# Optimization experiments

Measured on AMD Instinct MI355X. Metric: run time of the kernel, lower is better.

Reference implementation:

```python
import jax, jax.numpy as jnp
import numpy as np

B, T, C, H = 2, 2048, 1024, 16
HS = C // H                      # head_size = 64
LAYER_IDX = 2
LAMBDA_INIT = 0.8 - 0.6 * float(np.exp(-0.3 * (LAYER_IDX - 1)))
EPS = 1e-12


def setup_inputs() -> dict:
    key = jax.random.key(0)
    ks = jax.random.split(key, 22)
    std = 0.02
    w = lambda k, shape: (jax.random.normal(k, shape, jnp.float32) * std)
    inp = {
        'q': jax.random.normal(ks[0], (B, T, C), jnp.float32),
        'k': jax.random.normal(ks[1], (B, T, C), jnp.float32),
        'v': jax.random.normal(ks[2], (B, T, C), jnp.float32),
        'mask': jax.random.randint(ks[3], (B, T), 0, 2).astype(jnp.int32),
        # projection weights stored as (in, out) so y = x @ W + b
        'Wq1': w(ks[4], (C, C)), 'bq1': jnp.zeros((C,), jnp.float32),
        'Wq2': w(ks[5], (C, C)), 'bq2': jnp.zeros((C,), jnp.float32),
        'Wk1': w(ks[6], (C, C)), 'bk1': jnp.zeros((C,), jnp.float32),
        'Wk2': w(ks[7], (C, C)), 'bk2': jnp.zeros((C,), jnp.float32),
        'Wv':  w(ks[8], (C, 2 * C)), 'bv': jnp.zeros((2 * C,), jnp.float32),
        'Wc':  w(ks[9], (2 * C, C)), 'bc': jnp.zeros((C,), jnp.float32),
        'ln_w': jnp.ones((2 * HS,), jnp.float32),
        'ln_b': jnp.zeros((2 * HS,), jnp.float32),
        'lq1': jax.random.normal(ks[10], (H, HS), jnp.float32) * 0.1,
        'lk1': jax.random.normal(ks[11], (H, HS), jnp.float32) * 0.1,
        'lq2': jax.random.normal(ks[12], (H, HS), jnp.float32) * 0.1,
        'lk2': jax.random.normal(ks[13], (H, HS), jnp.float32) * 0.1,
    }
    return inp


def reference(q, k, v, mask, Wq1, bq1, Wq2, bq2, Wk1, bk1, Wk2, bk2,
              Wv, bv, Wc, bc, ln_w, ln_b, lq1, lk1, lq2, lk2):
    def heads(x, d):  # [B,T,H*d] -> [B,H,T,d]
        return x.reshape(B, T, H, d).transpose(0, 2, 1, 3)

    q1 = heads(q @ Wq1 + bq1, HS)
    q2 = heads(q @ Wq2 + bq2, HS)
    k1 = heads(k @ Wk1 + bk1, HS)
    k2 = heads(k @ Wk2 + bk2, HS)
    vv = heads(v @ Wv + bv, 2 * HS)          # [B,H,T,2*HS]

    scale = 1.0 / np.sqrt(HS)
    att1 = jnp.einsum('bhqd,bhkd->bhqk', q1, k1) * scale
    att2 = jnp.einsum('bhqd,bhkd->bhqk', q2, k2) * scale

    m = (mask == 0)[:, None, :, None]         # [B,1,Tq,1] -> masks query rows
    att1 = jnp.where(m, -1e9, att1)
    att2 = jnp.where(m, -1e9, att2)
    att1 = jax.nn.softmax(att1, axis=-1)
    att2 = jax.nn.softmax(att2, axis=-1)

    lam1 = jnp.exp(jnp.sum(lq1 * lk1, axis=-1))   # [H]
    lam2 = jnp.exp(jnp.sum(lq2 * lk2, axis=-1))
    lam = (lam1 - lam2 + LAMBDA_INIT)[None, :, None, None]
    att = att1 - lam * att2                       # differential attention

    y = jnp.einsum('bhqk,bhkd->bhqd', att, vv)    # [B,H,T,2*HS]

    # per-head TF-style LayerNorm over 2*HS, then (1 - lambda_init) scale
    u = y.mean(-1, keepdims=True)
    s = ((y - u) ** 2).mean(-1, keepdims=True)
    y = ln_w * ((y - u) / jnp.sqrt(s + EPS)) + ln_b
    y = y * (1.0 - LAMBDA_INIT)

    y = y.transpose(0, 2, 1, 3).reshape(B, T, 2 * C)
    return y @ Wc + bc
```

## Files before the change

### kernel.cpp

```cpp
#include <hip/hip_runtime.h>
#include <hip/hip_bf16.h>
#include <stdint.h>


#define T_SEQ 2048

typedef unsigned short u16;
typedef __attribute__((ext_vector_type(8))) short short8;
typedef __attribute__((ext_vector_type(4))) float f32x4;
typedef __attribute__((ext_vector_type(16))) float f32x16;

#define LAMBDA_INIT 0.35550906759096926f
#define ONE_MINUS_LI 0.6444909324090307f
#define SM_SCALE 0.125f
#define LOG2E 1.44269504f

__device__ __forceinline__ u16 f2bf(float f) {
  uint32_t u = __float_as_uint(f);
  return (u16)((u + 0x7FFFu + ((u >> 16) & 1u)) >> 16);
}
__device__ __forceinline__ float b2f(u16 u) {
  return __uint_as_float(((uint32_t)u) << 16);
}
__device__ __forceinline__ short8 ld8(const u16* p) {
  return *reinterpret_cast<const short8*>(p);
}
__device__ __forceinline__ void st8(u16* p, short8 v) {
  *reinterpret_cast<short8*>(p) = v;
}
__device__ __forceinline__ f32x4 mfma16(short8 a, short8 b, f32x4 c) {
  return __builtin_amdgcn_mfma_f32_16x16x32_bf16(a, b, c, 0, 0, 0);
}
__device__ __forceinline__ f32x16 mfma32(short8 a, short8 b, f32x16 c) {
  return __builtin_amdgcn_mfma_f32_32x32x16_bf16(a, b, c, 0, 0, 0);
}
__device__ __forceinline__ uint32_t cvtpk(float lo, float hi_) {
  uint32_t r;
  asm("v_cvt_pk_bf16_f32 %0, %1, %2" : "=v"(r) : "v"(lo), "v"(hi_));
  return r;
}

__global__ __launch_bounds__(256) void cvt_bf16(const float* __restrict__ in,
                                                u16* __restrict__ out, int n) {
  int i = (blockIdx.x * 256 + threadIdx.x) * 4;
  if (i >= n) return;
  float4 f = *reinterpret_cast<const float4*>(in + i);
  union { u16 u[4]; uint2 v; } pk;
  pk.u[0] = f2bf(f.x); pk.u[1] = f2bf(f.y); pk.u[2] = f2bf(f.z); pk.u[3] = f2bf(f.w);
  *reinterpret_cast<uint2*>(out + i) = pk.v;
}

__global__ __launch_bounds__(256) void tcvt(const float* __restrict__ W,
                                            u16* __restrict__ WT,
                                            int K, int N, int outRowOff) {
  __shared__ float tile[32][33];
  int n0 = blockIdx.x * 32, k0 = blockIdx.y * 32;
  int tx = threadIdx.x & 31, ty = threadIdx.x >> 5;
#pragma unroll
  for (int p = 0; p < 4; ++p)
    tile[ty + 8 * p][tx] = W[(size_t)(k0 + ty + 8 * p) * N + n0 + tx];
  __syncthreads();
#pragma unroll
  for (int p = 0; p < 4; ++p)
    WT[(size_t)(outRowOff + n0 + ty + 8 * p) * K + k0 + tx] = f2bf(tile[tx][ty + 8 * p]);
}

__global__ __launch_bounds__(256) void bias_concat(const float* __restrict__ b1,
                                                   const float* __restrict__ b2,
                                                   float* __restrict__ out) {
  int i = blockIdx.x * 256 + threadIdx.x;
  out[i] = (i < 1024) ? b1[i] : b2[i - 1024];
}

#define BM 128
#define BN 128
#define BK 64

template <int EPI>
__global__ __launch_bounds__(256) void gemm_bt(const u16* __restrict__ A,
                                               const u16* __restrict__ BT,
                                               const float* __restrict__ bias,
                                               void* __restrict__ Cv,
                                               int M, int N, int K) {
  __shared__ __align__(16) u16 As[BM * BK];
  __shared__ __align__(16) u16 Bs[BN * BK];
  int t = threadIdx.x;
  int w = t >> 6, l = t & 63;
  int g = l >> 4, c16 = l & 15;
  int wr = w >> 1, wc = w & 1;
  size_t gm = (size_t)blockIdx.y * BM, gn = (size_t)blockIdx.x * BN;

  f32x4 acc[4][4] = {};

  int srow = l >> 3;
  int scol = (l & 7) * 8;
  const u16* Ag = A + (gm + w * 32 + srow) * (size_t)K + scol;
  const u16* Bg = BT + (gn + w * 32 + srow) * (size_t)K + scol;

  for (int kt = 0; kt < K; kt += BK) {
    __syncthreads();
#pragma unroll
    for (int c = 0; c < 4; ++c) {
      __builtin_amdgcn_global_load_lds(
          (const __attribute__((address_space(1))) void*)(Ag + (size_t)(c * 8) * K + kt),
          (__attribute__((address_space(3))) void*)&As[(w * 32 + c * 8) * BK], 16, 0, 0);
      __builtin_amdgcn_global_load_lds(
          (const __attribute__((address_space(1))) void*)(Bg + (size_t)(c * 8) * K + kt),
          (__attribute__((address_space(3))) void*)&Bs[(w * 32 + c * 8) * BK], 16, 0, 0);
    }
    __syncthreads();
#pragma unroll
    for (int kk = 0; kk < 2; ++kk) {
      short8 af[4], bf[4];
#pragma unroll
      for (int m = 0; m < 4; ++m)
        af[m] = *reinterpret_cast<const short8*>(
            &As[(wr * 64 + m * 16 + c16) * BK + kk * 32 + g * 8]);
#pragma unroll
      for (int n = 0; n < 4; ++n)
        bf[n] = *reinterpret_cast<const short8*>(
            &Bs[(wc * 64 + n * 16 + c16) * BK + kk * 32 + g * 8]);
#pragma unroll
      for (int m = 0; m < 4; ++m)
#pragma unroll
        for (int n = 0; n < 4; ++n)
          acc[m][n] = mfma16(af[m], bf[n], acc[m][n]);
    }
  }

#pragma unroll
  for (int m = 0; m < 4; ++m)
#pragma unroll
    for (int n = 0; n < 4; ++n) {
      int row0 = (int)gm + wr * 64 + m * 16 + g * 4;
      int col = (int)gn + wc * 64 + n * 16 + c16;
      float bz = bias[col];
      if (EPI == 0) {
        u16* C = (u16*)Cv;
#pragma unroll
        for (int r = 0; r < 4; ++r)
          C[(size_t)(row0 + r) * N + col] = f2bf(acc[m][n][r] + bz);
      } else if (EPI == 1) {
        u16* C = (u16*)Cv;
        int bb = row0 >> 11, tt = row0 & 2047;
        union { u16 u[4]; uint2 v; } pk;
#pragma unroll
        for (int r = 0; r < 4; ++r) pk.u[r] = f2bf(acc[m][n][r] + bz);
        *reinterpret_cast<uint2*>(&C[((size_t)(bb * 2048 + col)) * 2048 + tt]) = pk.v;
      } else {
        float* C = (float*)Cv;
#pragma unroll
        for (int r = 0; r < 4; ++r)
          C[(size_t)(row0 + r) * N + col] = acc[m][n][r] + bz;
      }
    }
}

#define KROW 72
#define VROW 40
#define YROW 72
__global__ __launch_bounds__(256, 3) void diffattn(
    const u16* __restrict__ q1q2, const u16* __restrict__ k1k2,
    const u16* __restrict__ vvT, const int* __restrict__ mask,
    const float* __restrict__ lq1, const float* __restrict__ lk1,
    const float* __restrict__ lq2, const float* __restrict__ lk2,
    const float* __restrict__ lnw, const float* __restrict__ lnb,
    u16* __restrict__ yout) {
  __shared__ __align__(16) u16 smem[9728];
  u16* Ksm = smem;
  u16* Vsm = smem + 4608;
  u16* Ysm = smem;

  int tid = threadIdx.x;
  int w = tid >> 6, l = tid & 63;
  int q = l & 31, hi = l >> 5;
  int pair = w >> 1, stream = w & 1;

  int id = blockIdx.x;
  int j = id & 7, rest = id >> 3;
  int xblk = rest & 31, ygrp = rest >> 5;
  int bh = ygrp * 8 + j;
  int b = bh >> 4, h = bh & 15;
  int qr0 = xblk * 64 + pair * 32;

  float lm1 = lq1[h * 64 + l] * lk1[h * 64 + l];
  float lm2 = lq2[h * 64 + l] * lk2[h * 64 + l];
#pragma unroll
  for (int o = 32; o; o >>= 1) {
    lm1 += __shfl_xor(lm1, o);
    lm2 += __shfl_xor(lm2, o);
  }
  float lam = __expf(lm1) - __expf(lm2) + LAMBDA_INIT;

  int soff = stream * 1024;
  const u16* qrow = q1q2 + (size_t)(b * T_SEQ + qr0 + q) * 2048 + h * 64 + soff + hi * 8;
  short8 qf[4];
#pragma unroll
  for (int c = 0; c < 4; ++c) qf[c] = ld8(qrow + c * 16);

  float scale = (mask[b * T_SEQ + qr0 + q] == 0) ? 0.f : (SM_SCALE * LOG2E);

  float M = -INFINITY, L = 0.f;
  f32x16 acc[4] = {};

  int ku = tid * 2;
  int krow = ku >> 3, kslot = ku & 7;
  int kstream = krow >> 5, kkey = krow & 31;
  const u16* srcK = k1k2 + (size_t)(b * T_SEQ + kkey) * 2048 + h * 64 + kstream * 1024 + kslot * 8;
  u16* dstK = &Ksm[(kstream * 32 + kkey) * KROW + kslot * 8];
  int vd = tid >> 1, vslot = (tid & 1) * 2;
  const u16* srcV = vvT + ((size_t)(b * 16 + h) * 128 + vd) * 2048 + vslot * 8;
  u16* dstV = &Vsm[vd * VROW + vslot * 8];

  short8 kr0 = ld8(srcK), kr1 = ld8(srcK + 8);
  short8 vr0 = ld8(srcV), vr1 = ld8(srcV + 8);

  for (int kt = 0; kt < T_SEQ; kt += 32) {
    __syncthreads();
    st8(dstK, kr0); st8(dstK + 8, kr1);
    st8(dstV, vr0); st8(dstV + 8, vr1);
    __syncthreads();
    if (kt + 32 < T_SEQ) {
      const u16* nk = srcK + (size_t)(kt + 32) * 2048;
      kr0 = ld8(nk); kr1 = ld8(nk + 8);
      const u16* nv = srcV + (kt + 32);
      vr0 = ld8(nv); vr1 = ld8(nv + 8);
    }

    const u16* kbase = &Ksm[(stream * 32 + q) * KROW + hi * 8];
    short8 kf[4];
#pragma unroll
    for (int c = 0; c < 4; ++c) kf[c] = ld8(kbase + c * 16);

    f32x16 s = {};
#pragma unroll
    for (int c = 0; c < 4; ++c) s = mfma32(kf[c], qf[c], s);

    float rm = fmaxf(fmaxf(s[0], s[1]), s[2]);
    rm = fmaxf(fmaxf(rm, s[3]), s[4]);
    rm = fmaxf(fmaxf(rm, s[5]), s[6]);
    rm = fmaxf(fmaxf(rm, s[7]), s[8]);
    rm = fmaxf(fmaxf(rm, s[9]), s[10]);
    rm = fmaxf(fmaxf(rm, s[11]), s[12]);
    rm = fmaxf(fmaxf(rm, s[13]), s[14]);
    rm = fmaxf(rm, s[15]);
    rm = fmaxf(rm, __shfl_xor(rm, 32));
    float tm = rm * scale;

    if (!__all(tm - M <= 11.5f)) {
      float Mn = fmaxf(M, tm);
      float a = exp2f(M - Mn);
      L *= a;
#pragma unroll
      for (int d = 0; d < 4; ++d) acc[d] *= a;
      M = Mn;
    }

    float p[16];
#pragma unroll
    for (int r = 0; r < 16; ++r) p[r] = exp2f(__builtin_fmaf(s[r], scale, -M));
    float s8[8], s4[4];
#pragma unroll
    for (int i = 0; i < 8; ++i) s8[i] = p[i] + p[i + 8];
#pragma unroll
    for (int i = 0; i < 4; ++i) s4[i] = s8[i] + s8[i + 4];
    float ps = (s4[0] + s4[1]) + (s4[2] + s4[3]);
    ps += __shfl_xor(ps, 32);
    L += ps;

    uint32_t a1 = cvtpk(p[0], p[1]), a2 = cvtpk(p[2], p[3]);
    uint32_t b1 = cvtpk(p[4], p[5]), b2 = cvtpk(p[6], p[7]);
    uint32_t c1 = cvtpk(p[8], p[9]), c2 = cvtpk(p[10], p[11]);
    uint32_t d1 = cvtpk(p[12], p[13]), d2 = cvtpk(p[14], p[15]);
    uint32_t sa1 = (uint32_t)__shfl_xor((int)a1, 32), sa2 = (uint32_t)__shfl_xor((int)a2, 32);
    uint32_t sb1 = (uint32_t)__shfl_xor((int)b1, 32), sb2 = (uint32_t)__shfl_xor((int)b2, 32);
    uint32_t sc1 = (uint32_t)__shfl_xor((int)c1, 32), sc2 = (uint32_t)__shfl_xor((int)c2, 32);
    uint32_t sd1 = (uint32_t)__shfl_xor((int)d1, 32), sd2 = (uint32_t)__shfl_xor((int)d2, 32);
    union { uint32_t u[4]; short8 s8v; } pu0, pu1;
    pu0.u[0] = hi ? sb1 : a1;  pu0.u[1] = hi ? sb2 : a2;
    pu0.u[2] = hi ? b1 : sa1;  pu0.u[3] = hi ? b2 : sa2;
    pu1.u[0] = hi ? sd1 : c1;  pu1.u[1] = hi ? sd2 : c2;
    pu1.u[2] = hi ? d1 : sc1;  pu1.u[3] = hi ? d2 : sc2;
    short8 pf0 = pu0.s8v, pf1 = pu1.s8v;

#pragma unroll
    for (int d = 0; d < 4; ++d) {
      const u16* vb0 = &Vsm[(d * 32 + q) * VROW + hi * 8];
      short8 vf0 = ld8(vb0);
      short8 vf1 = ld8(vb0 + 16);
      acc[d] = mfma32(vf0, pf0, acc[d]);
      acc[d] = mfma32(vf1, pf1, acc[d]);
    }
  }

  float inv = 1.f / L;
  __syncthreads();
  if (stream == 1) {
    u16* yrow = &Ysm[(pair * 64 + l) * YROW];
#pragma unroll
    for (int d = 0; d < 4; ++d) {
      union { uint32_t u[8]; short8 v[2]; } pk;
#pragma unroll
      for (int i = 0; i < 8; ++i)
        pk.u[i] = cvtpk(acc[d][2 * i] * inv, acc[d][2 * i + 1] * inv);
      st8(yrow + d * 16, pk.v[0]);
      st8(yrow + d * 16 + 8, pk.v[1]);
    }
  }
  __syncthreads();
  if (stream == 0) {
    const u16* yrow = &Ysm[(pair * 64 + l) * YROW];
    float y[4][16];
#pragma unroll
    for (int d = 0; d < 4; ++d) {
      short8 y2a = ld8(yrow + d * 16);
      short8 y2b = ld8(yrow + d * 16 + 8);
#pragma unroll
      for (int i = 0; i < 8; ++i) {
        y[d][i] = acc[d][i] * inv - lam * b2f((u16)y2a[i]);
        y[d][8 + i] = acc[d][8 + i] * inv - lam * b2f((u16)y2b[i]);
      }
    }
    float sm = 0.f;
#pragma unroll
    for (int d = 0; d < 4; ++d)
#pragma unroll
      for (int r = 0; r < 16; ++r) sm += y[d][r];
    sm += __shfl_xor(sm, 32);
    float u = sm * (1.f / 128.f);
    float var = 0.f;
#pragma unroll
    for (int d = 0; d < 4; ++d)
#pragma unroll
      for (int r = 0; r < 16; ++r) { float dd = y[d][r] - u; var += dd * dd; }
    var += __shfl_xor(var, 32);
    float rstd = rsqrtf(var * (1.f / 128.f) + 1e-12f);

    size_t orow = (size_t)(b * T_SEQ + qr0 + q) * 2048 + h * 128;
#pragma unroll
    for (int d = 0; d < 4; ++d)
#pragma unroll
      for (int rr = 0; rr < 4; ++rr) {
        int base = d * 32 + 8 * rr + 4 * hi;
        union { u16 u[4]; uint2 v; } o;
#pragma unroll
        for (int i = 0; i < 4; ++i) {
          float yv = (lnw[base + i] * ((y[d][rr * 4 + i] - u) * rstd) + lnb[base + i]) *
                     ONE_MINUS_LI;
          o.u[i] = f2bf(yv);
        }
        *reinterpret_cast<uint2*>(&yout[orow + base]) = o.v;
      }
  }
}

extern "C" void kernel_launch(void* const* d_in, const int* in_sizes, int n_in,
                              void* d_out, int out_size, void* d_ws, size_t ws_size,
                              hipStream_t stream) {
  (void)in_sizes; (void)n_in; (void)out_size; (void)ws_size;
  const float* q   = (const float*)d_in[0];
  const float* k   = (const float*)d_in[1];
  const float* v   = (const float*)d_in[2];
  const int* maskp = (const int*)d_in[3];
  const float* Wq1 = (const float*)d_in[4];
  const float* bq1 = (const float*)d_in[5];
  const float* Wq2 = (const float*)d_in[6];
  const float* bq2 = (const float*)d_in[7];
  const float* Wk1 = (const float*)d_in[8];
  const float* bk1 = (const float*)d_in[9];
  const float* Wk2 = (const float*)d_in[10];
  const float* bk2 = (const float*)d_in[11];
  const float* Wv  = (const float*)d_in[12];
  const float* bv  = (const float*)d_in[13];
  const float* Wc  = (const float*)d_in[14];
  const float* bc  = (const float*)d_in[15];
  const float* lnw = (const float*)d_in[16];
  const float* lnb = (const float*)d_in[17];
  const float* lq1 = (const float*)d_in[18];
  const float* lk1 = (const float*)d_in[19];
  const float* lq2 = (const float*)d_in[20];
  const float* lk2 = (const float*)d_in[21];

  char* ws = (char*)d_ws;
  u16* qb     = (u16*)(ws + 0);
  u16* kb     = (u16*)(ws + 8388608);
  u16* vb     = (u16*)(ws + 16777216);
  u16* Wq12T  = (u16*)(ws + 25165824);
  u16* Wk12T  = (u16*)(ws + 29360128);
  u16* WvT    = (u16*)(ws + 33554432);
  u16* WcT    = (u16*)(ws + 37748736);
  float* biasq = (float*)(ws + 41943040);
  float* biask = (float*)(ws + 41951232);
  u16* q1q2   = (u16*)(ws + 41959424);
  u16* k1k2   = (u16*)(ws + 58736640);
  u16* vvT    = (u16*)(ws + 75513856);
  u16* yb     = (u16*)(ws + 0);

  const int NELEM = 2 * T_SEQ * 1024;

  cvt_bf16<<<4096, 256, 0, stream>>>(q, qb, NELEM);
  cvt_bf16<<<4096, 256, 0, stream>>>(k, kb, NELEM);
  cvt_bf16<<<4096, 256, 0, stream>>>(v, vb, NELEM);

  tcvt<<<dim3(32, 32), 256, 0, stream>>>(Wq1, Wq12T, 1024, 1024, 0);
  tcvt<<<dim3(32, 32), 256, 0, stream>>>(Wq2, Wq12T, 1024, 1024, 1024);
  tcvt<<<dim3(32, 32), 256, 0, stream>>>(Wk1, Wk12T, 1024, 1024, 0);
  tcvt<<<dim3(32, 32), 256, 0, stream>>>(Wk2, Wk12T, 1024, 1024, 1024);
  tcvt<<<dim3(64, 32), 256, 0, stream>>>(Wv, WvT, 1024, 2048, 0);
  tcvt<<<dim3(32, 64), 256, 0, stream>>>(Wc, WcT, 2048, 1024, 0);

  bias_concat<<<8, 256, 0, stream>>>(bq1, bq2, biasq);
  bias_concat<<<8, 256, 0, stream>>>(bk1, bk2, biask);

  gemm_bt<0><<<dim3(16, 32), 256, 0, stream>>>(qb, Wq12T, biasq, q1q2, 4096, 2048, 1024);
  gemm_bt<0><<<dim3(16, 32), 256, 0, stream>>>(kb, Wk12T, biask, k1k2, 4096, 2048, 1024);
  gemm_bt<1><<<dim3(16, 32), 256, 0, stream>>>(vb, WvT, bv, vvT, 4096, 2048, 1024);

  diffattn<<<1024, 256, 0, stream>>>(q1q2, k1k2, vvT, maskp,
                                     lq1, lk1, lq2, lk2, lnw, lnb, yb);

  gemm_bt<2><<<dim3(8, 32), 256, 0, stream>>>(yb, WcT, bc, d_out, 4096, 1024, 2048);
}
```

Before: 330.0 us.

## Merge Q/K projection GEMMs and stage 64-key K/V tiles in attention

The Q and K projection GEMMs become one launch over 8192 rows. Blocks in the second half offset the weight and bias pointers, which relies on the Q/K buffers, weights and biases sitting contiguously in the workspace. The attention kernel now stages 64 keys of K and V per barrier pair instead of 32, processing two 32-key sub-tiles per stage. This halves the syncthreads and prefetch rounds per key. In exchange, LDS per block roughly doubles and more registers are held in prefetch buffers, which may limit occupancy.

```diff
diff --git a/kernel.cpp b/kernel.cpp
--- a/kernel.cpp
+++ b/kernel.cpp
@@ -76,7 +76,7 @@
 #define BN 128
 #define BK 64
 
-template <int EPI>
+template <int EPI, bool QK>
 __global__ __launch_bounds__(256) void gemm_bt(const u16* __restrict__ A,
                                                const u16* __restrict__ BT,
                                                const float* __restrict__ bias,
@@ -89,6 +89,10 @@
   int g = l >> 4, c16 = l & 15;
   int wr = w >> 1, wc = w & 1;
   size_t gm = (size_t)blockIdx.y * BM, gn = (size_t)blockIdx.x * BN;
+  if (QK && gm >= 4096) {
+    BT += (size_t)2048 * 1024;
+    bias += 2048;
+  }
 
   f32x4 acc[4][4] = {};
 
@@ -157,7 +161,6 @@
 }
 
 #define KROW 72
-#define VROW 40
 #define YROW 72
 __global__ __launch_bounds__(256, 3) void diffattn(
     const u16* __restrict__ q1q2, const u16* __restrict__ k1k2,
@@ -166,9 +169,9 @@
     const float* __restrict__ lq2, const float* __restrict__ lk2,
     const float* __restrict__ lnw, const float* __restrict__ lnb,
     u16* __restrict__ yout) {
-  __shared__ __align__(16) u16 smem[9728];
+  __shared__ __align__(16) u16 smem[18432];
   u16* Ksm = smem;
-  u16* Vsm = smem + 4608;
+  u16* Vsm = smem + 9216;
   u16* Ysm = smem;
 
   int tid = threadIdx.x;
@@ -203,93 +206,105 @@
   float M = -INFINITY, L = 0.f;
   f32x16 acc[4] = {};
 
-  int ku = tid * 2;
-  int krow = ku >> 3, kslot = ku & 7;
-  int kstream = krow >> 5, kkey = krow & 31;
-  const u16* srcK = k1k2 + (size_t)(b * T_SEQ + kkey) * 2048 + h * 64 + kstream * 1024 + kslot * 8;
-  u16* dstK = &Ksm[(kstream * 32 + kkey) * KROW + kslot * 8];
-  int vd = tid >> 1, vslot = (tid & 1) * 2;
-  const u16* srcV = vvT + ((size_t)(b * 16 + h) * 128 + vd) * 2048 + vslot * 8;
-  u16* dstV = &Vsm[vd * VROW + vslot * 8];
-
-  short8 kr0 = ld8(srcK), kr1 = ld8(srcK + 8);
-  short8 vr0 = ld8(srcV), vr1 = ld8(srcV + 8);
-
-  for (int kt = 0; kt < T_SEQ; kt += 32) {
+  int srw = tid >> 1, shalf = tid & 1;
+  int kstream = srw >> 6, kkey = srw & 63;
+  const u16* srcK =
+      k1k2 + (size_t)(b * T_SEQ + kkey) * 2048 + h * 64 + kstream * 1024 + shalf * 32;
+  u16* dstK = &Ksm[srw * KROW + shalf * 32];
+  const u16* srcV = vvT + ((size_t)(b * 16 + h) * 128 + srw) * 2048 + shalf * 32;
+  u16* dstV = &Vsm[srw * KROW + shalf * 32];
+
+  short8 kpre[4], vpre[4];
+#pragma unroll
+  for (int u = 0; u < 4; ++u) {
+    kpre[u] = ld8(srcK + u * 8);
+    vpre[u] = ld8(srcV + u * 8);
+  }
+
+  for (int kt = 0; kt < T_SEQ; kt += 64) {
     __syncthreads();
-    st8(dstK, kr0); st8(dstK + 8, kr1);
-    st8(dstV, vr0); st8(dstV + 8, vr1);
+#pragma unroll
+    for (int u = 0; u < 4; ++u) {
+      st8(dstK + u * 8, kpre[u]);
+      st8(dstV + u * 8, vpre[u]);
+    }
     __syncthreads();
-    if (kt + 32 < T_SEQ) {
-      const u16* nk = srcK + (size_t)(kt + 32) * 2048;
-      kr0 = ld8(nk); kr1 = ld8(nk + 8);
-      const u16* nv = srcV + (kt + 32);
-      vr0 = ld8(nv); vr1 = ld8(nv + 8);
-    }
-
-    const u16* kbase = &Ksm[(stream * 32 + q) * KROW + hi * 8];
-    short8 kf[4];
-#pragma unroll
-    for (int c = 0; c < 4; ++c) kf[c] = ld8(kbase + c * 16);
-
-    f32x16 s = {};
-#pragma unroll
-    for (int c = 0; c < 4; ++c) s = mfma32(kf[c], qf[c], s);
-
-    float rm = fmaxf(fmaxf(s[0], s[1]), s[2]);
-    rm = fmaxf(fmaxf(rm, s[3]), s[4]);
-    rm = fmaxf(fmaxf(rm, s[5]), s[6]);
-    rm = fmaxf(fmaxf(rm, s[7]), s[8]);
-    rm = fmaxf(fmaxf(rm, s[9]), s[10]);
-    rm = fmaxf(fmaxf(rm, s[11]), s[12]);
-    rm = fmaxf(fmaxf(rm, s[13]), s[14]);
-    rm = fmaxf(rm, s[15]);
-    rm = fmaxf(rm, __shfl_xor(rm, 32));
-    float tm = rm * scale;
-
-    if (!__all(tm - M <= 11.5f)) {
-      float Mn = fmaxf(M, tm);
-      float a = exp2f(M - Mn);
-      L *= a;
-#pragma unroll
-      for (int d = 0; d < 4; ++d) acc[d] *= a;
-      M = Mn;
-    }
-
-    float p[16];
-#pragma unroll
-    for (int r = 0; r < 16; ++r) p[r] = exp2f(__builtin_fmaf(s[r], scale, -M));
-    float s8[8], s4[4];
-#pragma unroll
-    for (int i = 0; i < 8; ++i) s8[i] = p[i] + p[i + 8];
-#pragma unroll
-    for (int i = 0; i < 4; ++i) s4[i] = s8[i] + s8[i + 4];
-    float ps = (s4[0] + s4[1]) + (s4[2] + s4[3]);
-    ps += __shfl_xor(ps, 32);
-    L += ps;
-
-    uint32_t a1 = cvtpk(p[0], p[1]), a2 = cvtpk(p[2], p[3]);
-    uint32_t b1 = cvtpk(p[4], p[5]), b2 = cvtpk(p[6], p[7]);
-    uint32_t c1 = cvtpk(p[8], p[9]), c2 = cvtpk(p[10], p[11]);
-    uint32_t d1 = cvtpk(p[12], p[13]), d2 = cvtpk(p[14], p[15]);
-    uint32_t sa1 = (uint32_t)__shfl_xor((int)a1, 32), sa2 = (uint32_t)__shfl_xor((int)a2, 32);
-    uint32_t sb1 = (uint32_t)__shfl_xor((int)b1, 32), sb2 = (uint32_t)__shfl_xor((int)b2, 32);
-    uint32_t sc1 = (uint32_t)__shfl_xor((int)c1, 32), sc2 = (uint32_t)__shfl_xor((int)c2, 32);
-    uint32_t sd1 = (uint32_t)__shfl_xor((int)d1, 32), sd2 = (uint32_t)__shfl_xor((int)d2, 32);
-    union { uint32_t u[4]; short8 s8v; } pu0, pu1;
-    pu0.u[0] = hi ? sb1 : a1;  pu0.u[1] = hi ? sb2 : a2;
-    pu0.u[2] = hi ? b1 : sa1;  pu0.u[3] = hi ? b2 : sa2;
-    pu1.u[0] = hi ? sd1 : c1;  pu1.u[1] = hi ? sd2 : c2;
-    pu1.u[2] = hi ? d1 : sc1;  pu1.u[3] = hi ? d2 : sc2;
-    short8 pf0 = pu0.s8v, pf1 = pu1.s8v;
-
-#pragma unroll
-    for (int d = 0; d < 4; ++d) {
-      const u16* vb0 = &Vsm[(d * 32 + q) * VROW + hi * 8];
-      short8 vf0 = ld8(vb0);
-      short8 vf1 = ld8(vb0 + 16);
-      acc[d] = mfma32(vf0, pf0, acc[d]);
-      acc[d] = mfma32(vf1, pf1, acc[d]);
+    if (kt + 64 < T_SEQ) {
+      const u16* nk = srcK + (size_t)(kt + 64) * 2048;
+      const u16* nv = srcV + (kt + 64);
+#pragma unroll
+      for (int u = 0; u < 4; ++u) {
+        kpre[u] = ld8(nk + u * 8);
+        vpre[u] = ld8(nv + u * 8);
+      }
+    }
+
+#pragma unroll
+    for (int st = 0; st < 2; ++st) {
+      const u16* kbase = &Ksm[(stream * 64 + st * 32 + q) * KROW + hi * 8];
+      short8 kf[4];
+#pragma unroll
+      for (int c = 0; c < 4; ++c) kf[c] = ld8(kbase + c * 16);
+
+      f32x16 s = {};
+#pragma unroll
+      for (int c = 0; c < 4; ++c) s = mfma32(kf[c], qf[c], s);
+
+      float m0 = fmaxf(fmaxf(s[0], s[1]), s[2]);
+      float m1 = fmaxf(fmaxf(s[3], s[4]), s[5]);
+      float m2 = fmaxf(fmaxf(s[6], s[7]), s[8]);
+      float m3 = fmaxf(fmaxf(s[9], s[10]), s[11]);
+      float m4 = fmaxf(fmaxf(s[12], s[13]), s[14]);
+      float ma = fmaxf(fmaxf(m0, m1), m2);
+      float mb = fmaxf(fmaxf(m3, m4), s[15]);
+      float rm = fmaxf(ma, mb);
+      rm = fmaxf(rm, __shfl_xor(rm, 32));
+      float tm = rm * scale;
+
+      if (!__all(tm - M <= 11.5f)) {
+        float Mn = fmaxf(M, tm);
+        float a = exp2f(M - Mn);
+        L *= a;
+#pragma unroll
+        for (int d = 0; d < 4; ++d) acc[d] *= a;
+        M = Mn;
+      }
+
+      float p[16];
+#pragma unroll
+      for (int r = 0; r < 16; ++r) p[r] = exp2f(__builtin_fmaf(s[r], scale, -M));
+      float s8[8], s4[4];
+#pragma unroll
+      for (int i = 0; i < 8; ++i) s8[i] = p[i] + p[i + 8];
+#pragma unroll
+      for (int i = 0; i < 4; ++i) s4[i] = s8[i] + s8[i + 4];
+      float ps = (s4[0] + s4[1]) + (s4[2] + s4[3]);
+      ps += __shfl_xor(ps, 32);
+      L += ps;
+
+      uint32_t a1 = cvtpk(p[0], p[1]), a2 = cvtpk(p[2], p[3]);
+      uint32_t b1 = cvtpk(p[4], p[5]), b2 = cvtpk(p[6], p[7]);
+      uint32_t c1 = cvtpk(p[8], p[9]), c2 = cvtpk(p[10], p[11]);
+      uint32_t d1 = cvtpk(p[12], p[13]), d2 = cvtpk(p[14], p[15]);
+      uint32_t sa1 = (uint32_t)__shfl_xor((int)a1, 32), sa2 = (uint32_t)__shfl_xor((int)a2, 32);
+      uint32_t sb1 = (uint32_t)__shfl_xor((int)b1, 32), sb2 = (uint32_t)__shfl_xor((int)b2, 32);
+      uint32_t sc1 = (uint32_t)__shfl_xor((int)c1, 32), sc2 = (uint32_t)__shfl_xor((int)c2, 32);
+      uint32_t sd1 = (uint32_t)__shfl_xor((int)d1, 32), sd2 = (uint32_t)__shfl_xor((int)d2, 32);
+      union { uint32_t u[4]; short8 s8v; } pu0, pu1;
+      pu0.u[0] = hi ? sb1 : a1;  pu0.u[1] = hi ? sb2 : a2;
+      pu0.u[2] = hi ? b1 : sa1;  pu0.u[3] = hi ? b2 : sa2;
+      pu1.u[0] = hi ? sd1 : c1;  pu1.u[1] = hi ? sd2 : c2;
+      pu1.u[2] = hi ? d1 : sc1;  pu1.u[3] = hi ? d2 : sc2;
+      short8 pf0 = pu0.s8v, pf1 = pu1.s8v;
+
+#pragma unroll
+      for (int d = 0; d < 4; ++d) {
+        const u16* vb0 = &Vsm[(d * 32 + q) * KROW + st * 32 + hi * 8];
+        short8 vf0 = ld8(vb0);
+        short8 vf1 = ld8(vb0 + 16);
+        acc[d] = mfma32(vf0, pf0, acc[d]);
+        acc[d] = mfma32(vf1, pf1, acc[d]);
+      }
     }
   }
 
@@ -412,12 +427,12 @@
   bias_concat<<<8, 256, 0, stream>>>(bq1, bq2, biasq);
   bias_concat<<<8, 256, 0, stream>>>(bk1, bk2, biask);
 
-  gemm_bt<0><<<dim3(16, 32), 256, 0, stream>>>(qb, Wq12T, biasq, q1q2, 4096, 2048, 1024);
-  gemm_bt<0><<<dim3(16, 32), 256, 0, stream>>>(kb, Wk12T, biask, k1k2, 4096, 2048, 1024);
-  gemm_bt<1><<<dim3(16, 32), 256, 0, stream>>>(vb, WvT, bv, vvT, 4096, 2048, 1024);
+  gemm_bt<0, true><<<dim3(16, 64), 256, 0, stream>>>(qb, Wq12T, biasq, q1q2,
+                                                     8192, 2048, 1024);
+  gemm_bt<1, false><<<dim3(16, 32), 256, 0, stream>>>(vb, WvT, bv, vvT, 4096, 2048, 1024);
 
   diffattn<<<1024, 256, 0, stream>>>(q1q2, k1k2, vvT, maskp,
                                      lq1, lk1, lq2, lk2, lnw, lnb, yb);
 
-  gemm_bt<2><<<dim3(8, 32), 256, 0, stream>>>(yb, WcT, bc, d_out, 4096, 1024, 2048);
-}
+  gemm_bt<2, false><<<dim3(8, 32), 256, 0, stream>>>(yb, WcT, bc, d_out, 4096, 1024, 2048);
+}
```

New measurement: 327.7 us. Within noise of the previous version (-0.7%).
